# Optimization experiments

Hardware: AMD Instinct MI355X
Metric: run time of the kernel (lower is better)

The kernel has to match this reference:

```python
import jax, jax.numpy as jnp
import numpy as np

B, T, D, P, ALPHA, PR = 4, 4096, 1024, 512, 4, 64


def setup_inputs() -> dict:
    key = jax.random.key(0)
    ks = jax.random.split(key, 9)
    g = lambda k, shape, scale: jax.random.normal(k, shape, jnp.float32) * scale
    return {
        "x": jax.random.normal(ks[0], (B, T, D), jnp.float32),
        "W_toP": g(ks[1], (D, P), D ** -0.5),
        "W_U": g(ks[2], (D, P, ALPHA), D ** -0.5),
        "W_F": g(ks[3], (D, P), D ** -0.5),
        "W_V": g(ks[4], (P, ALPHA), 1.0),
        "W_lam": g(ks[5], (P, PR), P ** -0.5),
        "B_mat": g(ks[6], (P, PR), P ** -0.5),
        "C_mat": g(ks[7], (PR, P), PR ** -0.5),
        "W_fromP": g(ks[8], (P, D), P ** -0.5),
    }


def reference(x, W_toP, W_U, W_F, W_V, W_lam, B_mat, C_mat, W_fromP):
    # dense pre-path: (B,T,D)->(B,T,P)
    pre = jnp.einsum('btd,dp->btp', x, W_toP)
    # CeptaEmbedding dense pathway: multi-factor projection U, gates F, weighted Y
    U = jnp.einsum('btd,dpa->btpa', x, W_U)            # (B,T,P,alpha)
    Fg = jax.nn.sigmoid(jnp.einsum('btd,dp->btp', x, W_F))  # (B,T,P) in (0,1)
    Y = U * W_V                                        # (B,T,P,alpha)
    # CeptaRouting(reduce='sum'): sum over alpha factors, plus residual pre-path
    t = Y.sum(-1) + pre                                # (B,T,P)
    # CeptaSSMLowRank: input-dependent diagonal decay in rank-PR state space
    lam = jax.nn.sigmoid(jnp.einsum('btp,pr->btr', Fg, W_lam))  # (B,T,PR)
    u_in = jnp.einsum('btp,pr->btr', t, B_mat)                  # (B,T,PR)

    def step(s, inp):
        l, u = inp
        s = l * s + u
        return s, s

    s0 = jnp.zeros((x.shape[0], PR), x.dtype)
    _, s_seq = jax.lax.scan(step, s0, (lam.transpose(1, 0, 2), u_in.transpose(1, 0, 2)))
    s_seq = s_seq.transpose(1, 0, 2)                   # (B,T,PR)
    t_tilde = t + jnp.einsum('btr,rp->btp', s_seq, C_mat)
    h = jnp.einsum('btp,pd->btd', t_tilde, W_fromP)    # dropout p=0 -> identity
    return h
```

## Files before the change

kernel.cpp:

```cpp
#include <hip/hip_runtime.h>
#include <hip/hip_bf16.h>

#define Bb 4
#define Tt 4096
#define Dd 1024
#define Pp 512
#define PRr 64
#define Mm (Bb*Tt)
#define NCH 256
#define CL  16

typedef __bf16 bf16;
typedef __bf16 bf16x8 __attribute__((ext_vector_type(8)));
typedef __bf16 bf16x4 __attribute__((ext_vector_type(4)));
typedef float f32x4 __attribute__((ext_vector_type(4)));

#define GPTR(p) (const __attribute__((address_space(1))) void*)(p)
#define LPTR(p) (__attribute__((address_space(3))) void*)(p)

__device__ __forceinline__ float sigmoidf_(float x) {
    return 1.0f / (1.0f + __expf(-x));
}


__global__ void prep_w1(const float* __restrict__ W_toP, const float* __restrict__ W_U,
                        const float* __restrict__ W_V, const float* __restrict__ W_F,
                        bf16* __restrict__ W1t) {
    int idx = blockIdx.x * 256 + threadIdx.x;
    int n = idx >> 10, k = idx & 1023;
    float v;
    if (n < Pp) {
        int p = n;
        float4 u  = *(const float4*)(W_U + ((size_t)k * Pp + p) * 4);
        float4 wv = *(const float4*)(W_V + (size_t)p * 4);
        v = W_toP[(size_t)k * Pp + p] + u.x * wv.x + u.y * wv.y + u.z * wv.z + u.w * wv.w;
    } else {
        v = W_F[(size_t)k * Pp + (n - Pp)];
    }
    W1t[idx] = (bf16)v;
}

__global__ void prep_w3(const float* __restrict__ B_mat, const float* __restrict__ W_lam,
                        bf16* __restrict__ W3t, float* __restrict__ CW) {
    int bid = blockIdx.x;
    if (bid >= 512) {
        int i = (bid - 512) * 256 + threadIdx.x;
        ((f32x4*)CW)[i] = (f32x4){};
        return;
    }
    int idx = bid * 256 + threadIdx.x;
    int n = idx >> 10, k = idx & 1023;
    float v = 0.0f;
    if (n < PRr) { if (k < Pp) v = B_mat[(size_t)k * PRr + n]; }
    else         { if (k >= Pp) v = W_lam[(size_t)(k - Pp) * PRr + (n - PRr)]; }
    W3t[idx] = (bf16)v;
}

__global__ void prep_cw(const float* __restrict__ C_mat, const float* __restrict__ W_fromP,
                        float* __restrict__ CW) {
    __shared__ float crow[64];
    int nc = blockIdx.x;
    int r  = blockIdx.y;
    int pc = blockIdx.z;
    int tid = threadIdx.x;
    if (tid < 64) crow[tid] = C_mat[(size_t)r * Pp + pc * 64 + tid];
    __syncthreads();
    int n = nc * 256 + tid;
    float acc = 0.0f;
    #pragma unroll 8
    for (int i = 0; i < 64; ++i)
        acc = fmaf(crow[i], W_fromP[(size_t)(pc * 64 + i) * Dd + n], acc);
    atomicAdd(&CW[(size_t)r * Dd + n], acc);
}

__global__ void prep_w2(const float* __restrict__ W_fromP, const float* __restrict__ CW,
                        bf16* __restrict__ W2t) {
    int n = blockIdx.x;
    int k = threadIdx.x;
    float v = (k < Pp) ? W_fromP[(size_t)k * Dd + n]
                       : CW[(size_t)(k - Pp) * Dd + n];
    W2t[(size_t)n * 576 + k] = (bf16)v;
}

__global__ void scan_phase1(const float* __restrict__ UL,
                            float* __restrict__ slocal, float* __restrict__ pprod,
                            float* __restrict__ carryS, float* __restrict__ carryP) {
    int b = blockIdx.y;
    int c = blockIdx.x * 4 + (threadIdx.x >> 6);
    int r = threadIdx.x & 63;
    const float* ulb = UL + ((size_t)b * Tt + (size_t)c * CL) * 128;
    float* sl = slocal + ((size_t)b * Tt + (size_t)c * CL) * PRr;
    float* pp = pprod  + ((size_t)b * Tt + (size_t)c * CL) * PRr;
    float uv[CL], lv[CL];
    #pragma unroll
    for (int i = 0; i < CL; i++) {
        uv[i] = ulb[(size_t)i * 128 + r];
        lv[i] = ulb[(size_t)i * 128 + 64 + r];
    }
    float s = 0.0f, p = 1.0f;
    #pragma unroll
    for (int i = 0; i < CL; i++) {
        s = fmaf(lv[i], s, uv[i]);
        p *= lv[i];
        sl[(size_t)i * PRr + r] = s;
        pp[(size_t)i * PRr + r] = p;
    }
    int ci = b * NCH + c;
    carryS[(size_t)ci * PRr + r] = s;
    carryP[(size_t)ci * PRr + r] = p;
}

__global__ void scan_phase2(const float* __restrict__ carryS, const float* __restrict__ carryP,
                            float* __restrict__ carryIn) {
    int b = blockIdx.x, r = threadIdx.x;
    float carry = 0.0f;
    for (int c0 = 0; c0 < NCH; c0 += 16) {
        float cs[16], cp[16];
        #pragma unroll
        for (int i = 0; i < 16; i++) {
            size_t idx = ((size_t)b * NCH + c0 + i) * PRr + r;
            cs[i] = carryS[idx];
            cp[i] = carryP[idx];
        }
        #pragma unroll
        for (int i = 0; i < 16; i++) {
            carryIn[((size_t)b * NCH + c0 + i) * PRr + r] = carry;
            carry = fmaf(cp[i], carry, cs[i]);
        }
    }
}

__global__ void scan_phase3(const float* __restrict__ slocal, const float* __restrict__ pprod,
                            const float* __restrict__ carryIn, bf16* __restrict__ sb) {
    int i = blockIdx.x * 256 + threadIdx.x;
    int r = i & (PRr - 1);
    int row = i >> 6;
    int b = row >> 12;
    int t = row & (Tt - 1);
    int c = t / CL;
    float carry = carryIn[((size_t)b * NCH + c) * PRr + r];
    sb[i] = (bf16)fmaf(pprod[i], carry, slocal[i]);
}

template <int EPI, int AF32>
__global__ __launch_bounds__(512, 2) void gemm256(
    const bf16* __restrict__ A0, int lda0,
    const bf16* __restrict__ A1, int lda1, int ksplit,
    const float* __restrict__ Af,
    const bf16* __restrict__ Bt, int ldb, int K,
    void* __restrict__ Cout, int ldc, int sigcol) {

    __shared__ bf16 As[2][256 * 64];
    __shared__ bf16 Bs[2][256 * 64];

    const int tid  = threadIdx.x;
    const int lane = tid & 63;
    const int wid  = tid >> 6;
    const int wm   = wid >> 2;
    const int wn   = wid & 3;

    const int cpx = gridDim.x >> 3;
    const int bid = blockIdx.x;
    const int swz = (bid & 7) * cpx + (bid >> 3);
    const int mBase = (swz >> 2) * 256;
    const int nBase = (swz & 3) * 256;

    const int lr  = lane & 15;
    const int q16 = (lane >> 4) * 16;

    auto srcA = [&](int kt, const bf16*& src, int& lda, int& kc) {
        if (kt < ksplit) { src = A0; lda = lda0; kc = kt; }
        else             { src = A1; lda = lda1; kc = kt - ksplit; }
    };

    auto stage = [&](const bf16* src, int lda, int kc, int rowBase, bf16* lbuf, int rd) {
        int d = rd * 8192 + tid * 16;
        int L = d ^ (((d >> 7) & 7) << 4);
        int r = L >> 7;
        int c = (L & 127) >> 1;
        const bf16* g = src + (size_t)(rowBase + r) * lda + (kc + c);
        __builtin_amdgcn_global_load_lds(GPTR(g), LPTR((char*)lbuf + d), 16, 0, 0);
    };

    auto frag = [&](const bf16* lbuf, int r, int cb) -> bf16x8 {
        int flat = r * 128 + cb;
        int phys = flat ^ (((flat >> 7) & 7) << 4);
        return *(const bf16x8*)((const char*)lbuf + phys);
    };

    int rrA[4], ccA[4];
    #pragma unroll
    for (int rd = 0; rd < 4; ++rd) {
        int d = rd * 8192 + tid * 16;
        int L = d ^ (((d >> 7) & 7) << 4);
        rrA[rd] = L >> 7;
        ccA[rd] = (L & 127) >> 1;
    }
    f32x4 va[8];

    auto issueA = [&](int kc) {
        #pragma unroll
        for (int rd = 0; rd < 4; ++rd) {
            const float* g = Af + (size_t)(mBase + rrA[rd]) * Dd + kc + ccA[rd];
            va[2 * rd]     = *(const f32x4*)(g);
            va[2 * rd + 1] = *(const f32x4*)(g + 4);
        }
        asm volatile("" ::: "memory");
    };
    auto writeA = [&](bf16* lbuf) {
        #pragma unroll
        for (int rd = 0; rd < 4; ++rd) {
            bf16x8 o;
            #pragma unroll
            for (int j = 0; j < 4; ++j) {
                o[j]     = (bf16)va[2 * rd][j];
                o[j + 4] = (bf16)va[2 * rd + 1][j];
            }
            *(bf16x8*)((char*)lbuf + rd * 8192 + tid * 16) = o;
        }
    };

    const int NT = K / 64;

    if (AF32) {
        issueA(0);
        stage(Bt, ldb, 0, nBase, Bs[0], 0); stage(Bt, ldb, 0, nBase, Bs[0], 1);
        stage(Bt, ldb, 0, nBase, Bs[0], 2); stage(Bt, ldb, 0, nBase, Bs[0], 3);
        writeA(As[0]);
        asm volatile("s_waitcnt lgkmcnt(0)" ::: "memory");
        asm volatile("s_waitcnt vmcnt(0)" ::: "memory");
    } else {
        const bf16* sa; int la, kc; srcA(0, sa, la, kc);
        stage(sa, la, kc, mBase, As[0], 0); stage(sa, la, kc, mBase, As[0], 2);
        stage(Bt, ldb, 0, nBase, Bs[0], 0); stage(Bt, ldb, 0, nBase, Bs[0], 1);
        stage(Bt, ldb, 0, nBase, Bs[0], 2); stage(Bt, ldb, 0, nBase, Bs[0], 3);
        stage(sa, la, kc, mBase, As[0], 1); stage(sa, la, kc, mBase, As[0], 3);
        asm volatile("s_waitcnt vmcnt(2)" ::: "memory");
    }
    __builtin_amdgcn_s_barrier();

    f32x4 acc[8][4] = {};
    bf16x8 a[4], b0[4], b1[4];

    for (int t = 0; t < NT; ++t) {
        bf16* Ac = As[t & 1];       bf16* Bc = Bs[t & 1];
        bf16* An = As[(t + 1) & 1]; bf16* Bn = Bs[(t + 1) & 1];
        const bool hn = (t + 1 < NT);
        const bf16* sa = A0; int la = lda0, kc = 0;
        if (!AF32 && hn) srcA((t + 1) * 64, sa, la, kc);
        const int ktn = (t + 1) * 64;

        #pragma unroll
        for (int i = 0; i < 4; ++i) a[i]  = frag(Ac, wm * 128 + i * 16 + lr, q16);
        #pragma unroll
        for (int i = 0; i < 4; ++i) b0[i] = frag(Bc, wn * 64 + i * 16 + lr, q16);
        if (AF32) {
            if (hn) issueA(ktn);
        } else if (hn) {
            stage(sa, la, kc, mBase, An, 0); stage(sa, la, kc, mBase, An, 2);
            asm volatile("s_waitcnt vmcnt(2)" ::: "memory");
        } else {
            asm volatile("s_waitcnt vmcnt(0)" ::: "memory");
        }
        __builtin_amdgcn_s_barrier();
        __builtin_amdgcn_s_setprio(1);
        #pragma unroll
        for (int m = 0; m < 4; ++m)
            #pragma unroll
            for (int n = 0; n < 4; ++n)
                acc[m][n] = __builtin_amdgcn_mfma_f32_16x16x32_bf16(a[m], b0[n], acc[m][n], 0, 0, 0);
        __builtin_amdgcn_s_setprio(0);
        __builtin_amdgcn_s_barrier();

        #pragma unroll
        for (int i = 0; i < 4; ++i) a[i] = frag(Ac, wm * 128 + (i + 4) * 16 + lr, q16);
        if (hn) { stage(Bt, ldb, ktn, nBase, Bn, 0); stage(Bt, ldb, ktn, nBase, Bn, 1); }
        __builtin_amdgcn_s_barrier();
        __builtin_amdgcn_s_setprio(1);
        #pragma unroll
        for (int m = 0; m < 4; ++m)
            #pragma unroll
            for (int n = 0; n < 4; ++n)
                acc[m + 4][n] = __builtin_amdgcn_mfma_f32_16x16x32_bf16(a[m], b0[n], acc[m + 4][n], 0, 0, 0);
        __builtin_amdgcn_s_setprio(0);
        __builtin_amdgcn_s_barrier();

        #pragma unroll
        for (int i = 0; i < 4; ++i) a[i]  = frag(Ac, wm * 128 + i * 16 + lr, 64 + q16);
        #pragma unroll
        for (int i = 0; i < 4; ++i) b1[i] = frag(Bc, wn * 64 + i * 16 + lr, 64 + q16);
        if (hn) { stage(Bt, ldb, ktn, nBase, Bn, 2); stage(Bt, ldb, ktn, nBase, Bn, 3); }
        if (AF32 && hn) {
            writeA(An);
            asm volatile("s_waitcnt lgkmcnt(0)" ::: "memory");
        }
        __builtin_amdgcn_s_barrier();
        __builtin_amdgcn_s_setprio(1);
        #pragma unroll
        for (int m = 0; m < 4; ++m)
            #pragma unroll
            for (int n = 0; n < 4; ++n)
                acc[m][n] = __builtin_amdgcn_mfma_f32_16x16x32_bf16(a[m], b1[n], acc[m][n], 0, 0, 0);
        __builtin_amdgcn_s_setprio(0);
        __builtin_amdgcn_s_barrier();

        #pragma unroll
        for (int i = 0; i < 4; ++i) a[i] = frag(Ac, wm * 128 + (i + 4) * 16 + lr, 64 + q16);
        if (AF32) {
            if (hn) asm volatile("s_waitcnt vmcnt(0)" ::: "memory");
        } else if (hn) {
            stage(sa, la, kc, mBase, An, 1); stage(sa, la, kc, mBase, An, 3);
            asm volatile("s_waitcnt vmcnt(2)" ::: "memory");
        }
        __builtin_amdgcn_s_barrier();
        __builtin_amdgcn_s_setprio(1);
        #pragma unroll
        for (int m = 0; m < 4; ++m)
            #pragma unroll
            for (int n = 0; n < 4; ++n)
                acc[m + 4][n] = __builtin_amdgcn_mfma_f32_16x16x32_bf16(a[m], b1[n], acc[m + 4][n], 0, 0, 0);
        __builtin_amdgcn_s_setprio(0);
        __builtin_amdgcn_s_barrier();
    }

    const int lr4 = (lane >> 4) * 4;
    #pragma unroll
    for (int m = 0; m < 8; ++m) {
        #pragma unroll
        for (int n = 0; n < 4; ++n) {
            #pragma unroll
            for (int j = 0; j < 4; ++j) {
                int row = mBase + wm * 128 + m * 16 + lr4 + j;
                int col = nBase + wn * 64 + n * 16 + lr;
                float v = acc[m][n][j];
                if (EPI == 0) {
                    if (col >= sigcol) v = sigmoidf_(v);
                    ((bf16*)Cout)[(size_t)row * ldc + col] = (bf16)v;
                } else {
                    ((float*)Cout)[(size_t)row * ldc + col] = v;
                }
            }
        }
    }
}

template <int EPI>
__global__ __launch_bounds__(256) void gemm_bt(
    const bf16* __restrict__ A0, int lda0,
    const bf16* __restrict__ A1, int lda1, int ksplit,
    const bf16* __restrict__ Bt, int K,
    void* __restrict__ Cout, int ldc, int sigcol) {

    __shared__ bf16 As[128][32];
    __shared__ bf16 Bs[128][32];

    const int tid  = threadIdx.x;
    const int lane = tid & 63;
    const int wid  = tid >> 6;
    const int wr   = (wid >> 1) * 64;
    const int wc   = (wid & 1) * 64;
    const int mBase = blockIdx.x * 128;
    const int nBase = blockIdx.y * 128;

    f32x4 acc[4][4] = {};

    const int lr = lane & 15;
    const int lk = (lane >> 4) * 8;

    for (int kt = 0; kt < K; kt += 32) {
        const bf16* Asrc; int lda_; int kcol;
        if (kt < ksplit) { Asrc = A0; lda_ = lda0; kcol = kt; }
        else             { Asrc = A1; lda_ = lda1; kcol = kt - ksplit; }

        __syncthreads();
        #pragma unroll
        for (int i = 0; i < 2; i++) {
            int c = tid + i * 256;
            int row = c >> 2, k8 = (c & 3) * 8;
            const bf16* g = Asrc + (size_t)(mBase + row) * lda_ + (kcol + k8);
            __builtin_amdgcn_global_load_lds(GPTR(g), LPTR(&As[0][0] + c * 8), 16, 0, 0);
        }
        #pragma unroll
        for (int i = 0; i < 2; i++) {
            int c = tid + i * 256;
            int row = c >> 2, k8 = (c & 3) * 8;
            const bf16* g = Bt + (size_t)(nBase + row) * K + (kt + k8);
            __builtin_amdgcn_global_load_lds(GPTR(g), LPTR(&Bs[0][0] + c * 8), 16, 0, 0);
        }
        __syncthreads();

        bf16x8 af[4], bfr[4];
        #pragma unroll
        for (int m = 0; m < 4; m++) af[m]  = *(const bf16x8*)(&As[wr + m * 16 + lr][lk]);
        #pragma unroll
        for (int n = 0; n < 4; n++) bfr[n] = *(const bf16x8*)(&Bs[wc + n * 16 + lr][lk]);
        #pragma unroll
        for (int m = 0; m < 4; m++)
            #pragma unroll
            for (int n = 0; n < 4; n++)
                acc[m][n] = __builtin_amdgcn_mfma_f32_16x16x32_bf16(af[m], bfr[n], acc[m][n], 0, 0, 0);
    }

    const int lr4 = (lane >> 4) * 4;
    const int lc  = lane & 15;
    #pragma unroll
    for (int m = 0; m < 4; m++) {
        #pragma unroll
        for (int n = 0; n < 4; n++) {
            #pragma unroll
            for (int j = 0; j < 4; j++) {
                int row = mBase + wr + m * 16 + lr4 + j;
                int col = nBase + wc + n * 16 + lc;
                float v = acc[m][n][j];
                if (EPI == 1) {
                    if (col >= sigcol) v = sigmoidf_(v);
                    ((float*)Cout)[(size_t)row * ldc + col] = v;
                } else {
                    ((float*)Cout)[(size_t)row * ldc + col] = v;
                }
            }
        }
    }
}

extern "C" void kernel_launch(void* const* d_in, const int* in_sizes, int n_in,
                              void* d_out, int out_size, void* d_ws, size_t ws_size,
                              hipStream_t stream) {
    const float* x       = (const float*)d_in[0];
    const float* W_toP   = (const float*)d_in[1];
    const float* W_U     = (const float*)d_in[2];
    const float* W_F     = (const float*)d_in[3];
    const float* W_V     = (const float*)d_in[4];
    const float* W_lam   = (const float*)d_in[5];
    const float* B_mat   = (const float*)d_in[6];
    const float* C_mat   = (const float*)d_in[7];
    const float* W_fromP = (const float*)d_in[8];
    float* out = (float*)d_out;

    char* ws = (char*)d_ws;
    size_t off = 0;
    auto alloc = [&](size_t bytes) { void* p = ws + off; off = (off + bytes + 255) & ~255ULL; return p; };
    bf16*  TF  = (bf16*)alloc((size_t)Mm * 1024 * 2);
    float* UL  = (float*)alloc((size_t)Mm * 128 * 4);
    bf16*  sb  = (bf16*)alloc((size_t)Mm * PRr * 2);
    bf16*  W1t = (bf16*)alloc((size_t)1024 * 1024 * 2);
    bf16*  W3t = (bf16*)alloc((size_t)128 * 1024 * 2);
    bf16*  W2t = (bf16*)alloc((size_t)1024 * 576 * 2);
    float* CW  = (float*)alloc((size_t)PRr * Dd * 4);
    float* slocal = (float*)alloc((size_t)Mm * PRr * 4);
    float* pprod  = (float*)alloc((size_t)Mm * PRr * 4);
    float* carryS = (float*)alloc((size_t)Bb * NCH * PRr * 4);
    float* carryP = (float*)alloc((size_t)Bb * NCH * PRr * 4);
    float* carryI = (float*)alloc((size_t)Bb * NCH * PRr * 4);

    prep_w1<<<dim3(4096), dim3(256), 0, stream>>>(W_toP, W_U, W_V, W_F, W1t);
    prep_w3<<<dim3(576),  dim3(256), 0, stream>>>(B_mat, W_lam, W3t, CW);
    prep_cw<<<dim3(4, 64, 8), dim3(256), 0, stream>>>(C_mat, W_fromP, CW);
    prep_w2<<<dim3(1024), dim3(576), 0, stream>>>(W_fromP, CW, W2t);

    gemm256<0, 1><<<dim3((Mm / 256) * (1024 / 256)), 512, 0, stream>>>(
        nullptr, 0, nullptr, 0, 1 << 30, x, W1t, Dd, Dd, TF, 1024, Pp);

    gemm_bt<1><<<dim3(Mm / 128, 1), 256, 0, stream>>>(
        TF, 1024, TF, 1024, 1 << 30, W3t, 1024, UL, 128, PRr);

    scan_phase1<<<dim3(NCH / 4, Bb), dim3(256), 0, stream>>>(UL, slocal, pprod, carryS, carryP);
    scan_phase2<<<dim3(Bb), dim3(PRr), 0, stream>>>(carryS, carryP, carryI);
    scan_phase3<<<dim3(Mm * PRr / 256), dim3(256), 0, stream>>>(slocal, pprod, carryI, sb);

    gemm256<2, 0><<<dim3((Mm / 256) * (1024 / 256)), 512, 0, stream>>>(
        TF, 1024, sb, PRr, Pp, nullptr, W2t, 576, 576, out, Dd, 1 << 30);
}
```

Baseline: 149.1 us.

## Double-buffer fp32 A-tile register prefetch two K-tiles ahead in GEMM

In the path where A is fp32, the GEMM now keeps two register buffers and alternates them. Each iteration loads the A tile two K-steps ahead while the next tile is converted to bf16 and written to LDS. B staging for the next tile moves earlier in the iteration, and the vmcnt waits are relaxed so only the older loads must finish. The aim is to hide global-load latency for the fp32 activations, at the cost of 32 extra VGPRs per thread, which may lower occupancy. The loop is also unrolled by two, which assumes an even K-tile count.

```diff
diff --git a/kernel.cpp b/kernel.cpp
--- a/kernel.cpp
+++ b/kernel.cpp
@@ -196,25 +196,25 @@
         rrA[rd] = L >> 7;
         ccA[rd] = (L & 127) >> 1;
     }
-    f32x4 va[8];
-
-    auto issueA = [&](int kc) {
+    f32x4 vaA[8], vaB[8];
+
+    auto issueA = [&](f32x4 (&v)[8], int kc) {
         #pragma unroll
         for (int rd = 0; rd < 4; ++rd) {
             const float* g = Af + (size_t)(mBase + rrA[rd]) * Dd + kc + ccA[rd];
-            va[2 * rd]     = *(const f32x4*)(g);
-            va[2 * rd + 1] = *(const f32x4*)(g + 4);
+            v[2 * rd]     = *(const f32x4*)(g);
+            v[2 * rd + 1] = *(const f32x4*)(g + 4);
         }
         asm volatile("" ::: "memory");
     };
-    auto writeA = [&](bf16* lbuf) {
+    auto writeA = [&](f32x4 (&v)[8], bf16* lbuf) {
         #pragma unroll
         for (int rd = 0; rd < 4; ++rd) {
             bf16x8 o;
             #pragma unroll
             for (int j = 0; j < 4; ++j) {
-                o[j]     = (bf16)va[2 * rd][j];
-                o[j + 4] = (bf16)va[2 * rd + 1][j];
+                o[j]     = (bf16)v[2 * rd][j];
+                o[j + 4] = (bf16)v[2 * rd + 1][j];
             }
             *(bf16x8*)((char*)lbuf + rd * 8192 + tid * 16) = o;
         }
@@ -223,12 +223,17 @@
     const int NT = K / 64;
 
     if (AF32) {
-        issueA(0);
+        issueA(vaA, 0);
         stage(Bt, ldb, 0, nBase, Bs[0], 0); stage(Bt, ldb, 0, nBase, Bs[0], 1);
         stage(Bt, ldb, 0, nBase, Bs[0], 2); stage(Bt, ldb, 0, nBase, Bs[0], 3);
-        writeA(As[0]);
+        writeA(vaA, As[0]);
         asm volatile("s_waitcnt lgkmcnt(0)" ::: "memory");
-        asm volatile("s_waitcnt vmcnt(0)" ::: "memory");
+        if (NT > 1) {
+            issueA(vaB, 64);
+            asm volatile("s_waitcnt vmcnt(8)" ::: "memory");
+        } else {
+            asm volatile("s_waitcnt vmcnt(0)" ::: "memory");
+        }
     } else {
         const bf16* sa; int la, kc; srcA(0, sa, la, kc);
         stage(sa, la, kc, mBase, As[0], 0); stage(sa, la, kc, mBase, As[0], 2);
@@ -242,10 +247,11 @@
     f32x4 acc[8][4] = {};
     bf16x8 a[4], b0[4], b1[4];
 
-    for (int t = 0; t < NT; ++t) {
+    auto tile = [&](int t, f32x4 (&vwr)[8], f32x4 (&vis)[8]) {
         bf16* Ac = As[t & 1];       bf16* Bc = Bs[t & 1];
         bf16* An = As[(t + 1) & 1]; bf16* Bn = Bs[(t + 1) & 1];
-        const bool hn = (t + 1 < NT);
+        const bool hn  = (t + 1 < NT);
+        const bool hn2 = (t + 2 < NT);
         const bf16* sa = A0; int la = lda0, kc = 0;
         if (!AF32 && hn) srcA((t + 1) * 64, sa, la, kc);
         const int ktn = (t + 1) * 64;
@@ -255,7 +261,7 @@
         #pragma unroll
         for (int i = 0; i < 4; ++i) b0[i] = frag(Bc, wn * 64 + i * 16 + lr, q16);
         if (AF32) {
-            if (hn) issueA(ktn);
+            if (hn) { stage(Bt, ldb, ktn, nBase, Bn, 0); stage(Bt, ldb, ktn, nBase, Bn, 1); }
         } else if (hn) {
             stage(sa, la, kc, mBase, An, 0); stage(sa, la, kc, mBase, An, 2);
             asm volatile("s_waitcnt vmcnt(2)" ::: "memory");
@@ -274,7 +280,11 @@
 
         #pragma unroll
         for (int i = 0; i < 4; ++i) a[i] = frag(Ac, wm * 128 + (i + 4) * 16 + lr, q16);
-        if (hn) { stage(Bt, ldb, ktn, nBase, Bn, 0); stage(Bt, ldb, ktn, nBase, Bn, 1); }
+        if (AF32) {
+            if (hn) { stage(Bt, ldb, ktn, nBase, Bn, 2); stage(Bt, ldb, ktn, nBase, Bn, 3); }
+        } else if (hn) {
+            stage(Bt, ldb, ktn, nBase, Bn, 0); stage(Bt, ldb, ktn, nBase, Bn, 1);
+        }
         __builtin_amdgcn_s_barrier();
         __builtin_amdgcn_s_setprio(1);
         #pragma unroll
@@ -289,10 +299,12 @@
         for (int i = 0; i < 4; ++i) a[i]  = frag(Ac, wm * 128 + i * 16 + lr, 64 + q16);
         #pragma unroll
         for (int i = 0; i < 4; ++i) b1[i] = frag(Bc, wn * 64 + i * 16 + lr, 64 + q16);
-        if (hn) { stage(Bt, ldb, ktn, nBase, Bn, 2); stage(Bt, ldb, ktn, nBase, Bn, 3); }
-        if (AF32 && hn) {
-            writeA(An);
-            asm volatile("s_waitcnt lgkmcnt(0)" ::: "memory");
+        if (AF32) {
+            if (hn) writeA(vwr, An);
+            if (hn2) issueA(vis, (t + 2) * 64);
+            if (hn) asm volatile("s_waitcnt lgkmcnt(0)" ::: "memory");
+        } else if (hn) {
+            stage(Bt, ldb, ktn, nBase, Bn, 2); stage(Bt, ldb, ktn, nBase, Bn, 3);
         }
         __builtin_amdgcn_s_barrier();
         __builtin_amdgcn_s_setprio(1);
@@ -307,7 +319,10 @@
         #pragma unroll
         for (int i = 0; i < 4; ++i) a[i] = frag(Ac, wm * 128 + (i + 4) * 16 + lr, 64 + q16);
         if (AF32) {
-            if (hn) asm volatile("s_waitcnt vmcnt(0)" ::: "memory");
+            if (hn) {
+                if (hn2) asm volatile("s_waitcnt vmcnt(8)" ::: "memory");
+                else     asm volatile("s_waitcnt vmcnt(0)" ::: "memory");
+            }
         } else if (hn) {
             stage(sa, la, kc, mBase, An, 1); stage(sa, la, kc, mBase, An, 3);
             asm volatile("s_waitcnt vmcnt(2)" ::: "memory");
@@ -321,6 +336,15 @@
                 acc[m + 4][n] = __builtin_amdgcn_mfma_f32_16x16x32_bf16(a[m], b1[n], acc[m + 4][n], 0, 0, 0);
         __builtin_amdgcn_s_setprio(0);
         __builtin_amdgcn_s_barrier();
+    };
+
+    if (AF32) {
+        for (int t = 0; t < NT; t += 2) {
+            tile(t,     vaB, vaA);
+            tile(t + 1, vaA, vaB);
+        }
+    } else {
+        for (int t = 0; t < NT; ++t) tile(t, vaA, vaA);
     }
 
     const int lr4 = (lane >> 4) * 4;
```

Result: slower. 308.3 us (+106.8%).

## Prefetch fp32 A tiles two K-steps ahead using split register halves

Applied to the files above, without the earlier changes.

In the fp32-A GEMM path, the A tile is now split into two register halves that are loaded from global memory two K-iterations ahead, then converted to bf16 and written to LDS one iteration ahead. The goal is to hide global load latency instead of waiting on vmcnt(0) within each iteration. The B staging for the next tile is moved earlier in the iteration. This increases register pressure and makes the vmcnt bookkeeping more intricate. The bf16-A path is split into its own loop but is otherwise unchanged.

```diff
diff --git a/kernel.cpp b/kernel.cpp
--- a/kernel.cpp
+++ b/kernel.cpp
@@ -196,39 +196,42 @@
         rrA[rd] = L >> 7;
         ccA[rd] = (L & 127) >> 1;
     }
-    f32x4 va[8];
-
-    auto issueA = [&](int kc) {
-        #pragma unroll
-        for (int rd = 0; rd < 4; ++rd) {
-            const float* g = Af + (size_t)(mBase + rrA[rd]) * Dd + kc + ccA[rd];
-            va[2 * rd]     = *(const f32x4*)(g);
-            va[2 * rd + 1] = *(const f32x4*)(g + 4);
+    f32x4 H0[4], H1[4];
+
+    auto issueH = [&](f32x4 (&v)[4], int kc, int rdb) {
+        #pragma unroll
+        for (int rd = 0; rd < 2; ++rd) {
+            const float* g = Af + (size_t)(mBase + rrA[rdb + rd]) * Dd + kc + ccA[rdb + rd];
+            v[2 * rd]     = *(const f32x4*)(g);
+            v[2 * rd + 1] = *(const f32x4*)(g + 4);
         }
         asm volatile("" ::: "memory");
     };
-    auto writeA = [&](bf16* lbuf) {
-        #pragma unroll
-        for (int rd = 0; rd < 4; ++rd) {
+    auto writeH = [&](f32x4 (&v)[4], bf16* lbuf, int rdb) {
+        #pragma unroll
+        for (int rd = 0; rd < 2; ++rd) {
             bf16x8 o;
             #pragma unroll
             for (int j = 0; j < 4; ++j) {
-                o[j]     = (bf16)va[2 * rd][j];
-                o[j + 4] = (bf16)va[2 * rd + 1][j];
+                o[j]     = (bf16)v[2 * rd][j];
+                o[j + 4] = (bf16)v[2 * rd + 1][j];
             }
-            *(bf16x8*)((char*)lbuf + rd * 8192 + tid * 16) = o;
+            *(bf16x8*)((char*)lbuf + (rdb + rd) * 8192 + tid * 16) = o;
         }
     };
 
     const int NT = K / 64;
 
     if (AF32) {
-        issueA(0);
+        issueH(H0, 0, 0); issueH(H1, 0, 2);
         stage(Bt, ldb, 0, nBase, Bs[0], 0); stage(Bt, ldb, 0, nBase, Bs[0], 1);
         stage(Bt, ldb, 0, nBase, Bs[0], 2); stage(Bt, ldb, 0, nBase, Bs[0], 3);
-        writeA(As[0]);
+        writeH(H0, As[0], 0);
+        writeH(H1, As[0], 2);
+        if (NT > 1) { issueH(H0, 64, 0); issueH(H1, 64, 2); }
         asm volatile("s_waitcnt lgkmcnt(0)" ::: "memory");
-        asm volatile("s_waitcnt vmcnt(0)" ::: "memory");
+        if (NT > 1) asm volatile("s_waitcnt vmcnt(8)" ::: "memory");
+        else        asm volatile("s_waitcnt vmcnt(0)" ::: "memory");
     } else {
         const bf16* sa; int la, kc; srcA(0, sa, la, kc);
         stage(sa, la, kc, mBase, As[0], 0); stage(sa, la, kc, mBase, As[0], 2);
@@ -242,86 +245,128 @@
     f32x4 acc[8][4] = {};
     bf16x8 a[4], b0[4], b1[4];
 
-    for (int t = 0; t < NT; ++t) {
-        bf16* Ac = As[t & 1];       bf16* Bc = Bs[t & 1];
-        bf16* An = As[(t + 1) & 1]; bf16* Bn = Bs[(t + 1) & 1];
-        const bool hn = (t + 1 < NT);
-        const bf16* sa = A0; int la = lda0, kc = 0;
-        if (!AF32 && hn) srcA((t + 1) * 64, sa, la, kc);
-        const int ktn = (t + 1) * 64;
-
-        #pragma unroll
-        for (int i = 0; i < 4; ++i) a[i]  = frag(Ac, wm * 128 + i * 16 + lr, q16);
-        #pragma unroll
-        for (int i = 0; i < 4; ++i) b0[i] = frag(Bc, wn * 64 + i * 16 + lr, q16);
-        if (AF32) {
-            if (hn) issueA(ktn);
-        } else if (hn) {
-            stage(sa, la, kc, mBase, An, 0); stage(sa, la, kc, mBase, An, 2);
-            asm volatile("s_waitcnt vmcnt(2)" ::: "memory");
-        } else {
-            asm volatile("s_waitcnt vmcnt(0)" ::: "memory");
-        }
-        __builtin_amdgcn_s_barrier();
-        __builtin_amdgcn_s_setprio(1);
-        #pragma unroll
-        for (int m = 0; m < 4; ++m)
-            #pragma unroll
-            for (int n = 0; n < 4; ++n)
-                acc[m][n] = __builtin_amdgcn_mfma_f32_16x16x32_bf16(a[m], b0[n], acc[m][n], 0, 0, 0);
-        __builtin_amdgcn_s_setprio(0);
-        __builtin_amdgcn_s_barrier();
-
-        #pragma unroll
-        for (int i = 0; i < 4; ++i) a[i] = frag(Ac, wm * 128 + (i + 4) * 16 + lr, q16);
-        if (hn) { stage(Bt, ldb, ktn, nBase, Bn, 0); stage(Bt, ldb, ktn, nBase, Bn, 1); }
-        __builtin_amdgcn_s_barrier();
-        __builtin_amdgcn_s_setprio(1);
-        #pragma unroll
-        for (int m = 0; m < 4; ++m)
-            #pragma unroll
-            for (int n = 0; n < 4; ++n)
-                acc[m + 4][n] = __builtin_amdgcn_mfma_f32_16x16x32_bf16(a[m], b0[n], acc[m + 4][n], 0, 0, 0);
-        __builtin_amdgcn_s_setprio(0);
-        __builtin_amdgcn_s_barrier();
-
-        #pragma unroll
-        for (int i = 0; i < 4; ++i) a[i]  = frag(Ac, wm * 128 + i * 16 + lr, 64 + q16);
-        #pragma unroll
-        for (int i = 0; i < 4; ++i) b1[i] = frag(Bc, wn * 64 + i * 16 + lr, 64 + q16);
-        if (hn) { stage(Bt, ldb, ktn, nBase, Bn, 2); stage(Bt, ldb, ktn, nBase, Bn, 3); }
-        if (AF32 && hn) {
-            writeA(An);
-            asm volatile("s_waitcnt lgkmcnt(0)" ::: "memory");
-        }
-        __builtin_amdgcn_s_barrier();
-        __builtin_amdgcn_s_setprio(1);
-        #pragma unroll
-        for (int m = 0; m < 4; ++m)
-            #pragma unroll
-            for (int n = 0; n < 4; ++n)
-                acc[m][n] = __builtin_amdgcn_mfma_f32_16x16x32_bf16(a[m], b1[n], acc[m][n], 0, 0, 0);
-        __builtin_amdgcn_s_setprio(0);
-        __builtin_amdgcn_s_barrier();
-
-        #pragma unroll
-        for (int i = 0; i < 4; ++i) a[i] = frag(Ac, wm * 128 + (i + 4) * 16 + lr, 64 + q16);
-        if (AF32) {
-            if (hn) asm volatile("s_waitcnt vmcnt(0)" ::: "memory");
-        } else if (hn) {
-            stage(sa, la, kc, mBase, An, 1); stage(sa, la, kc, mBase, An, 3);
-            asm volatile("s_waitcnt vmcnt(2)" ::: "memory");
-        }
-        __builtin_amdgcn_s_barrier();
-        __builtin_amdgcn_s_setprio(1);
-        #pragma unroll
-        for (int m = 0; m < 4; ++m)
-            #pragma unroll
-            for (int n = 0; n < 4; ++n)
-                acc[m + 4][n] = __builtin_amdgcn_mfma_f32_16x16x32_bf16(a[m], b1[n], acc[m + 4][n], 0, 0, 0);
-        __builtin_amdgcn_s_setprio(0);
-        __builtin_amdgcn_s_barrier();
-    }
+#define MFMA16(AOFF, AV, BV)                                                          \
+    _Pragma("unroll")                                                                 \
+    for (int m_ = 0; m_ < 4; ++m_)                                                    \
+        _Pragma("unroll")                                                             \
+        for (int n_ = 0; n_ < 4; ++n_)                                                \
+            acc[m_ + AOFF][n_] = __builtin_amdgcn_mfma_f32_16x16x32_bf16(             \
+                AV[m_], BV[n_], acc[m_ + AOFF][n_], 0, 0, 0);
+
+    if (AF32) {
+        for (int t = 0; t < NT; ++t) {
+            bf16* Ac = As[t & 1];       bf16* Bc = Bs[t & 1];
+            bf16* An = As[(t + 1) & 1]; bf16* Bn = Bs[(t + 1) & 1];
+            const bool hn  = (t + 1 < NT);
+            const bool hn2 = (t + 2 < NT);
+            const int ktn  = (t + 1) * 64;
+            const int ktn2 = (t + 2) * 64;
+
+            #pragma unroll
+            for (int i = 0; i < 4; ++i) a[i]  = frag(Ac, wm * 128 + i * 16 + lr, q16);
+            #pragma unroll
+            for (int i = 0; i < 4; ++i) b0[i] = frag(Bc, wn * 64 + i * 16 + lr, q16);
+            if (hn) { stage(Bt, ldb, ktn, nBase, Bn, 0); stage(Bt, ldb, ktn, nBase, Bn, 1); }
+            __builtin_amdgcn_s_barrier();
+            __builtin_amdgcn_s_setprio(1);
+            MFMA16(0, a, b0)
+            __builtin_amdgcn_s_setprio(0);
+            __builtin_amdgcn_s_barrier();
+
+            #pragma unroll
+            for (int i = 0; i < 4; ++i) a[i] = frag(Ac, wm * 128 + (i + 4) * 16 + lr, q16);
+            if (hn) { stage(Bt, ldb, ktn, nBase, Bn, 2); stage(Bt, ldb, ktn, nBase, Bn, 3); }
+            __builtin_amdgcn_s_barrier();
+            __builtin_amdgcn_s_setprio(1);
+            MFMA16(4, a, b0)
+            __builtin_amdgcn_s_setprio(0);
+            __builtin_amdgcn_s_barrier();
+
+            #pragma unroll
+            for (int i = 0; i < 4; ++i) a[i]  = frag(Ac, wm * 128 + i * 16 + lr, 64 + q16);
+            #pragma unroll
+            for (int i = 0; i < 4; ++i) b1[i] = frag(Bc, wn * 64 + i * 16 + lr, 64 + q16);
+            if (hn)  writeH(H0, An, 0);
+            if (hn2) issueH(H0, ktn2, 0);
+            if (hn)  asm volatile("s_waitcnt lgkmcnt(0)" ::: "memory");
+            __builtin_amdgcn_s_barrier();
+            __builtin_amdgcn_s_setprio(1);
+            MFMA16(0, a, b1)
+            __builtin_amdgcn_s_setprio(0);
+            __builtin_amdgcn_s_barrier();
+
+            #pragma unroll
+            for (int i = 0; i < 4; ++i) a[i] = frag(Ac, wm * 128 + (i + 4) * 16 + lr, 64 + q16);
+            if (hn)  writeH(H1, An, 2);
+            if (hn2) issueH(H1, ktn2, 2);
+            if (hn)  asm volatile("s_waitcnt lgkmcnt(0)" ::: "memory");
+            if (hn2)      asm volatile("s_waitcnt vmcnt(8)" ::: "memory");
+            else if (hn)  asm volatile("s_waitcnt vmcnt(0)" ::: "memory");
+            __builtin_amdgcn_s_barrier();
+            __builtin_amdgcn_s_setprio(1);
+            MFMA16(4, a, b1)
+            __builtin_amdgcn_s_setprio(0);
+            __builtin_amdgcn_s_barrier();
+        }
+    } else {
+        for (int t = 0; t < NT; ++t) {
+            bf16* Ac = As[t & 1];       bf16* Bc = Bs[t & 1];
+            bf16* An = As[(t + 1) & 1]; bf16* Bn = Bs[(t + 1) & 1];
+            const bool hn = (t + 1 < NT);
+            const bf16* sa = A0; int la = lda0, kc = 0;
+            if (hn) srcA((t + 1) * 64, sa, la, kc);
+            const int ktn = (t + 1) * 64;
+
+            #pragma unroll
+            for (int i = 0; i < 4; ++i) a[i]  = frag(Ac, wm * 128 + i * 16 + lr, q16);
+            #pragma unroll
+            for (int i = 0; i < 4; ++i) b0[i] = frag(Bc, wn * 64 + i * 16 + lr, q16);
+            if (hn) {
+                stage(sa, la, kc, mBase, An, 0); stage(sa, la, kc, mBase, An, 2);
+                asm volatile("s_waitcnt vmcnt(2)" ::: "memory");
+            } else {
+                asm volatile("s_waitcnt vmcnt(0)" ::: "memory");
+            }
+            __builtin_amdgcn_s_barrier();
+            __builtin_amdgcn_s_setprio(1);
+            MFMA16(0, a, b0)
+            __builtin_amdgcn_s_setprio(0);
+            __builtin_amdgcn_s_barrier();
+
+            #pragma unroll
+            for (int i = 0; i < 4; ++i) a[i] = frag(Ac, wm * 128 + (i + 4) * 16 + lr, q16);
+            if (hn) { stage(Bt, ldb, ktn, nBase, Bn, 0); stage(Bt, ldb, ktn, nBase, Bn, 1); }
+            __builtin_amdgcn_s_barrier();
+            __builtin_amdgcn_s_setprio(1);
+            MFMA16(4, a, b0)
+            __builtin_amdgcn_s_setprio(0);
+            __builtin_amdgcn_s_barrier();
+
+            #pragma unroll
+            for (int i = 0; i < 4; ++i) a[i]  = frag(Ac, wm * 128 + i * 16 + lr, 64 + q16);
+            #pragma unroll
+            for (int i = 0; i < 4; ++i) b1[i] = frag(Bc, wn * 64 + i * 16 + lr, 64 + q16);
+            if (hn) { stage(Bt, ldb, ktn, nBase, Bn, 2); stage(Bt, ldb, ktn, nBase, Bn, 3); }
+            __builtin_amdgcn_s_barrier();
+            __builtin_amdgcn_s_setprio(1);
+            MFMA16(0, a, b1)
+            __builtin_amdgcn_s_setprio(0);
+            __builtin_amdgcn_s_barrier();
+
+            #pragma unroll
+            for (int i = 0; i < 4; ++i) a[i] = frag(Ac, wm * 128 + (i + 4) * 16 + lr, 64 + q16);
+            if (hn) {
+                stage(sa, la, kc, mBase, An, 1); stage(sa, la, kc, mBase, An, 3);
+                asm volatile("s_waitcnt vmcnt(2)" ::: "memory");
+            }
+            __builtin_amdgcn_s_barrier();
+            __builtin_amdgcn_s_setprio(1);
+            MFMA16(4, a, b1)
+            __builtin_amdgcn_s_setprio(0);
+            __builtin_amdgcn_s_barrier();
+        }
+    }
+#undef MFMA16
 
     const int lr4 = (lane >> 4) * 4;
     #pragma unroll
```

Measured after the change: 145.4 us. 2.5% less time.
